# Kernel optimization log

Hardware: AMD Instinct MI355X
Metric: run time of the kernel (lower is better)

## Reference

```python
import jax, jax.numpy as jnp
import numpy as np

B, S, E, H = 2, 2048, 4096, 32
D = E // H  # head_dim = 128
MAX_SEQ = 2048


def precompute_freqs(dim, end, theta=10000.0):
    # Faithful to the torch source, including its operator precedence:
    # freqs = 1.0 / (theta ** arange(0, dim, 2)[:dim//2].float() / dim)
    # i.e. 1.0 / ((theta ** exps) / dim); overflows to inf in fp32 -> freq 0.
    exps = jnp.arange(0, dim, 2, dtype=jnp.float32)[: dim // 2]
    freqs = 1.0 / (jnp.power(jnp.float32(theta), exps) / jnp.float32(dim))
    t = jnp.arange(end, dtype=jnp.float32)
    f = jnp.outer(t, freqs)  # [end, dim//2]
    return jnp.cos(f), jnp.sin(f)


def apply_rope(x, cos, sin, pos):
    # x: [B,H,S,D]; cos/sin: [max_seq, dim//2]; pos: [B,S]
    c = cos[pos][:, None]  # [B,1,S,f]
    s = sin[pos][:, None]
    xr = x.reshape(*x.shape[:-1], -1, 2)  # [B,H,S,D/2,2]
    x1, x2 = xr[..., 0], xr[..., 1]
    if x1.shape[-1] > c.shape[-1]:
        rep = x1.shape[-1] // c.shape[-1]  # repeat_interleave factor
        c = jnp.repeat(c, rep, axis=-1)
        s = jnp.repeat(s, rep, axis=-1)
    out = jnp.stack([x1 * c - x2 * s, x1 * s + x2 * c], axis=-1)
    return out.reshape(x.shape)


def setup_inputs() -> dict:
    key = jax.random.key(0)
    kx, kq, kk, kv, ko = jax.random.split(key, 5)
    x = jax.random.normal(kx, (B, S, E), jnp.float32)
    scale = 0.02
    Wq = jax.random.normal(kq, (E, E), jnp.float32) * scale
    Wk = jax.random.normal(kk, (E, E), jnp.float32) * scale
    Wv = jax.random.normal(kv, (E, E), jnp.float32) * scale
    Wo = jax.random.normal(ko, (E, E), jnp.float32) * scale
    z = jnp.zeros((E,), jnp.float32)
    return {"x": x, "Wq": Wq, "bq": z, "Wk": Wk, "bk": z, "Wv": Wv, "bv": z, "Wo": Wo, "bo": z}


def reference(x, Wq, bq, Wk, bk, Wv, bv, Wo, bo):
    cos, sin = precompute_freqs(H, MAX_SEQ)  # note: dim = n_heads, as in source
    pos = jnp.broadcast_to(jnp.arange(S)[None, :], (B, S))  # no offset, S <= max
    # QKV projections (torch Linear: x @ W.T + b)
    q = (x @ Wq.T + bq).reshape(B, S, H, D).transpose(0, 2, 1, 3)  # [B,H,S,D]
    k = (x @ Wk.T + bk).reshape(B, S, H, D).transpose(0, 2, 1, 3)
    v = (x @ Wv.T + bv).reshape(B, S, H, D).transpose(0, 2, 1, 3)
    q = apply_rope(q, cos, sin, pos)
    k = apply_rope(k, cos, sin, pos)
    # SDPA with mask=None (non-causal, full attention)
    scores = jnp.einsum("bhqd,bhkd->bhqk", q, k) / np.float32(np.sqrt(D))
    att = jax.nn.softmax(scores, axis=-1)
    out = jnp.einsum("bhqk,bhkd->bhqd", att, v)
    out = out.transpose(0, 2, 1, 3).reshape(B, S, E)
    return out @ Wo.T + bo
```

## Files before the change

kernel.cpp:

```cpp
#include <hip/hip_runtime.h>
#include <math.h>

typedef _Float16 half8 __attribute__((ext_vector_type(8)));
typedef _Float16 half4 __attribute__((ext_vector_type(4)));
typedef __fp16 fp16x2 __attribute__((ext_vector_type(2)));
typedef float f32x4 __attribute__((ext_vector_type(4)));
typedef unsigned uint4v __attribute__((ext_vector_type(4)));

struct FreqT { float f[16]; };

__device__ __forceinline__ f32x4 mfma16(half8 a, half8 b, f32x4 c) {
  return __builtin_amdgcn_mfma_f32_16x16x32_f16(a, b, c, 0, 0, 0);
}

__device__ __forceinline__ void gload_lds16(const void* g, void* l) {
  __builtin_amdgcn_global_load_lds(
      (const __attribute__((address_space(1))) void*)g,
      (__attribute__((address_space(3))) void*)l, 16, 0, 0);
}

__device__ __forceinline__ unsigned pk_f16(float p0, float p1) {
  fp16x2 h = __builtin_amdgcn_cvt_pkrtz(p0, p1);
  return __builtin_bit_cast(unsigned, h);
}

#define S_BARRIER() __builtin_amdgcn_s_barrier()
#define WAIT_LGKM0() asm volatile("s_waitcnt lgkmcnt(0)" ::: "memory")
#define WAIT_VM8() asm volatile("s_waitcnt vmcnt(8)" ::: "memory")
#define WAIT_VM4() asm volatile("s_waitcnt vmcnt(4)" ::: "memory")
#define WAIT_VM0() asm volatile("s_waitcnt vmcnt(0)" ::: "memory")

__global__ __launch_bounds__(256)
void cast_f32_f16(const float* __restrict__ in, _Float16* __restrict__ out, long n8) {
  long i = (long)blockIdx.x * blockDim.x + threadIdx.x;
  if (i >= n8) return;
  float4 a = ((const float4*)in)[2 * i];
  float4 b = ((const float4*)in)[2 * i + 1];
  half8 v;
  v[0] = (_Float16)a.x; v[1] = (_Float16)a.y; v[2] = (_Float16)a.z; v[3] = (_Float16)a.w;
  v[4] = (_Float16)b.x; v[5] = (_Float16)b.y; v[6] = (_Float16)b.z; v[7] = (_Float16)b.w;
  ((half8*)out)[i] = v;
}

#define GBM 256
#define GBN 256
#define GBK 64

template <typename OutT>
__global__ __launch_bounds__(512, 2)
void gemm256(const _Float16* __restrict__ A, const _Float16* __restrict__ W,
             const float* __restrict__ bias, OutT* __restrict__ C,
             int M, int N, int K) {
  __shared__ __align__(16) _Float16 lds[4][GBM * GBK];

  int nwg = gridDim.x;
  int bid = blockIdx.x;
  int cpx = nwg >> 3;
  int swz = (bid & 7) * cpx + (bid >> 3);
  int ntn = N / GBN;
  int m0 = (swz / ntn) * GBM, n0 = (swz % ntn) * GBN;

  int tid = threadIdx.x, lane = tid & 63, w = tid >> 6;
  int wm = w >> 2, wn = w & 3;
  int g = lane >> 4, lc = lane & 15;

  int r8 = w * 8 + (lane >> 3);
  int cs = (((lane & 7) ^ (lane >> 3)) << 3);
  const _Float16* gA = A + (size_t)(m0 + r8) * K + cs;
  const _Float16* gB = W + (size_t)(n0 + r8) * K + cs;

#define STAGE(bi, k0) do {                                            \
    _Float16* la_ = &lds[(bi) * 2][0] + w * 512;                      \
    _Float16* lb_ = &lds[(bi) * 2 + 1][0] + w * 512;                  \
    _Pragma("unroll")                                                 \
    for (int i_ = 0; i_ < 4; ++i_) {                                  \
      gload_lds16(gA + (size_t)(i_ * 64) * K + (k0), la_ + i_ * 4096);\
      gload_lds16(gB + (size_t)(i_ * 64) * K + (k0), lb_ + i_ * 4096);\
    } } while (0)

  int aOff[8], bOff[4];
#pragma unroll
  for (int mf = 0; mf < 8; ++mf) aOff[mf] = (wm * 128 + mf * 16 + lc) * 64;
#pragma unroll
  for (int nf = 0; nf < 4; ++nf) bOff[nf] = (wn * 64 + nf * 16 + lc) * 64;
  int co0 = (((0 * 4 + g) ^ (lc & 7)) << 3);
  int co1 = (((1 * 4 + g) ^ (lc & 7)) << 3);

  half8 a0[8], a1[8], b0[4], b1[4];
  f32x4 acc[8][4] = {};

#define LOAD_SET0(bi) do {                                            \
    const _Float16* lA_ = &lds[(bi) * 2][0];                          \
    const _Float16* lB_ = &lds[(bi) * 2 + 1][0];                      \
    _Pragma("unroll")                                                 \
    for (int mf = 0; mf < 4; ++mf) {                                  \
      a0[mf * 2 + 0] = *(const half8*)&lA_[aOff[mf] + co0];           \
      a0[mf * 2 + 1] = *(const half8*)&lA_[aOff[mf] + co1];           \
    }                                                                 \
    _Pragma("unroll")                                                 \
    for (int nf = 0; nf < 2; ++nf) {                                  \
      b0[nf * 2 + 0] = *(const half8*)&lB_[bOff[nf] + co0];           \
      b0[nf * 2 + 1] = *(const half8*)&lB_[bOff[nf] + co1];           \
    } } while (0)

#define LOAD_SET1(bi) do {                                            \
    const _Float16* lA_ = &lds[(bi) * 2][0];                          \
    const _Float16* lB_ = &lds[(bi) * 2 + 1][0];                      \
    _Pragma("unroll")                                                 \
    for (int mf = 0; mf < 4; ++mf) {                                  \
      a1[mf * 2 + 0] = *(const half8*)&lA_[aOff[mf + 4] + co0];       \
      a1[mf * 2 + 1] = *(const half8*)&lA_[aOff[mf + 4] + co1];       \
    }                                                                 \
    _Pragma("unroll")                                                 \
    for (int nf = 0; nf < 2; ++nf) {                                  \
      b1[nf * 2 + 0] = *(const half8*)&lB_[bOff[nf + 2] + co0];       \
      b1[nf * 2 + 1] = *(const half8*)&lB_[bOff[nf + 2] + co1];       \
    } } while (0)

#define MFMA_Q(mq, nq, ar, br) do {                                   \
    __builtin_amdgcn_s_setprio(1);                                    \
    _Pragma("unroll")                                                 \
    for (int mf = 0; mf < 4; ++mf)                                    \
      _Pragma("unroll")                                               \
      for (int nf = 0; nf < 2; ++nf)                                  \
        _Pragma("unroll")                                             \
        for (int kk = 0; kk < 2; ++kk)                                \
          acc[(mq) * 4 + mf][(nq) * 2 + nf] =                         \
              mfma16(ar[mf * 2 + kk], br[nf * 2 + kk],                \
                     acc[(mq) * 4 + mf][(nq) * 2 + nf]);              \
    __builtin_amdgcn_s_setprio(0); } while (0)

  const int NT = K >> 6;

  STAGE(0, 0);
  STAGE(1, GBK);
  WAIT_VM8();
  S_BARRIER();
  LOAD_SET0(0);

  for (int t = 0; t < NT - 2; ++t) {
    int cur = t & 1;
    LOAD_SET1(cur);
    MFMA_Q(0, 0, a0, b0);
    MFMA_Q(0, 1, a0, b1);
    WAIT_LGKM0();
    S_BARRIER();
    STAGE(cur, (t + 2) << 6);
    MFMA_Q(1, 1, a1, b1);
    MFMA_Q(1, 0, a1, b0);
    WAIT_VM8();
    S_BARRIER();
    LOAD_SET0(cur ^ 1);
  }
  {
    int cur = (NT - 2) & 1;
    LOAD_SET1(cur);
    MFMA_Q(0, 0, a0, b0);
    MFMA_Q(0, 1, a0, b1);
    MFMA_Q(1, 1, a1, b1);
    MFMA_Q(1, 0, a1, b0);
    WAIT_VM0();
    S_BARRIER();
    LOAD_SET0(cur ^ 1);
  }
  {
    LOAD_SET1((NT - 1) & 1);
    MFMA_Q(0, 0, a0, b0);
    MFMA_Q(0, 1, a0, b1);
    MFMA_Q(1, 1, a1, b1);
    MFMA_Q(1, 0, a1, b0);
  }

  int crow = m0 + wm * 128 + g * 4;
  int ccol = n0 + wn * 64 + lc;
#pragma unroll
  for (int nf = 0; nf < 4; ++nf) {
    float bv = bias[ccol + nf * 16];
#pragma unroll
    for (int mf = 0; mf < 8; ++mf)
#pragma unroll
      for (int j = 0; j < 4; ++j)
        C[(size_t)(crow + mf * 16 + j) * N + ccol + nf * 16] =
            (OutT)(acc[mf][nf][j] + bv);
  }
#undef STAGE
#undef LOAD_SET0
#undef LOAD_SET1
#undef MFMA_Q
}

__global__ __launch_bounds__(256)
void rope_kernel(_Float16* __restrict__ x, FreqT ft, int Sn, int E, long n8) {
  long i = (long)blockIdx.x * blockDim.x + threadIdx.x;
  if (i >= n8) return;
  int epr = E / 8;
  int e8 = (int)(i % epr);
  int s = (int)((i / epr) % Sn);
  int fj = e8 & 15;
  float fr = ft.f[fj];
  float ang = (float)s * fr;
  float sv, cv;
  sincosf(ang, &sv, &cv);
  half8 v = ((const half8*)x)[i];
  half8 o;
#pragma unroll
  for (int p = 0; p < 4; ++p) {
    float x1 = (float)v[2 * p], x2 = (float)v[2 * p + 1];
    o[2 * p] = (_Float16)(x1 * cv - x2 * sv);
    o[2 * p + 1] = (_Float16)(x1 * sv + x2 * cv);
  }
  ((half8*)x)[i] = o;
}

__global__ __launch_bounds__(256)
void transpose_v(const _Float16* __restrict__ v, _Float16* __restrict__ vt,
                 int Hn, int Sn) {
  const int D = 128;
  const int E = Hn * D;
  __shared__ _Float16 t[64][130];
  int spb = Sn / 64;
  int bid = blockIdx.x;
  int s0 = (bid % spb) * 64;
  int bh = bid / spb;
  int b = bh / Hn, h = bh % Hn;
  int tid = threadIdx.x;
  int r = tid >> 2, dc = (tid & 3) * 32;
  const _Float16* src = v + (size_t)(b * Sn + s0 + r) * E + h * D + dc;
#pragma unroll
  for (int i = 0; i < 4; ++i) {
    half8 x = *(const half8*)(src + i * 8);
#pragma unroll
    for (int k = 0; k < 4; ++k) {
      _Float16 a0 = x[2 * k], a1 = x[2 * k + 1];
      t[r][dc + i * 8 + 2 * k] = a0;
      t[r][dc + i * 8 + 2 * k + 1] = a1;
    }
  }
  __syncthreads();
  int d = tid >> 1, sh = (tid & 1) * 32;
  half8 ov[4];
#pragma unroll
  for (int c = 0; c < 4; ++c)
#pragma unroll
    for (int j = 0; j < 8; ++j)
      ov[c][j] = t[sh + c * 8 + j][d];
  _Float16* dst = vt + ((size_t)bh * D + d) * Sn + s0 + sh;
#pragma unroll
  for (int c = 0; c < 4; ++c)
    *(half8*)(dst + c * 8) = ov[c];
}

#define QB 128
#define KB 64

__global__ __launch_bounds__(256, 2)
void flash_attn(const _Float16* __restrict__ qg, const _Float16* __restrict__ kg,
                const _Float16* __restrict__ vt, _Float16* __restrict__ og,
                int Bn, int Hn, int Sn) {
  const int D = 128;
  const int E = Hn * D;

  __shared__ _Float16 Ksh[2][KB * 128];
  __shared__ _Float16 Vsh[D * KB];
  __shared__ float sm[4][32];

  int qtiles = Sn / QB;
  int bid = blockIdx.x;
  int bh = bid / qtiles, qt = bid % qtiles;
  int b = bh / Hn, h = bh % Hn;

  int tid = threadIdx.x, lane = tid & 63, w = tid >> 6;
  int g = lane >> 4, lc = lane & 15;
  int lc7 = lc & 7;

  const size_t headoff = ((size_t)b * Sn) * E + (size_t)h * D;
  const _Float16* qp = qg + headoff;
  const _Float16* kp = kg + headoff;
  const _Float16* vtp = vt + (size_t)(b * Hn + h) * D * Sn;

  int q0 = qt * QB + w * 32;
  half8 aq[2][4];
#pragma unroll
  for (int mf = 0; mf < 2; ++mf)
#pragma unroll
    for (int kf = 0; kf < 4; ++kf)
      aq[mf][kf] = *(const half8*)(qp + (size_t)(q0 + mf * 16 + lc) * E + kf * 32 + g * 8);

  float mrun[2] = {-1e30f, -1e30f}, lpart[2] = {0.f, 0.f};
  f32x4 o[2][8] = {};

  const float scale = 0.08838834764831845f;

  int krow = 4 * w + (lane >> 4);
  int kcol = ((lane & 15) ^ (krow & 7)) * 8;
  const _Float16* gK = kp + (size_t)krow * E + kcol;
  int vrow = w * 32 + (lane >> 3);
  int vcol = ((lane & 7) ^ (vrow & 7)) * 8;
  const _Float16* gV = vtp + (size_t)vrow * Sn + vcol;

  float* smw = sm[w];

  const int NT = Sn / KB;

  {
    _Float16* lK = Ksh[0] + w * 512;
#pragma unroll
    for (int i = 0; i < 4; ++i)
      gload_lds16(gK + (size_t)(16 * i) * E, lK + i * 2048);
  }
  WAIT_VM0();
  S_BARRIER();

  for (int t = 0; t < NT; ++t) {
    int c = t & 1;
    {
      _Float16* lV = Vsh + w * 2048;
#pragma unroll
      for (int p = 0; p < 4; ++p)
        gload_lds16(gV + (size_t)(p * 8) * Sn + t * KB, lV + p * 512);
    }
    if (t + 1 < NT) {
      _Float16* lK = Ksh[c ^ 1] + w * 512;
#pragma unroll
      for (int i = 0; i < 4; ++i)
        gload_lds16(gK + (size_t)((t + 1) * KB + 16 * i) * E, lK + i * 2048);
    }

    f32x4 st[2][4] = {};
    {
      const _Float16* Kc = Ksh[c];
      __builtin_amdgcn_s_setprio(1);
#pragma unroll
      for (int kf = 0; kf < 4; ++kf) {
        half8 bk[4];
#pragma unroll
        for (int nf = 0; nf < 4; ++nf)
          bk[nf] = *(const half8*)&Kc[(nf * 16 + lc) * 128 + (((kf * 4 + g) ^ lc7) << 3)];
#pragma unroll
        for (int nf = 0; nf < 4; ++nf)
#pragma unroll
          for (int mf = 0; mf < 2; ++mf)
            st[mf][nf] = mfma16(bk[nf], aq[mf][kf], st[mf][nf]);
      }
      __builtin_amdgcn_s_setprio(0);
    }

    bool resc[2];
#pragma unroll
    for (int mf = 0; mf < 2; ++mf) {
      f32x4 m4 = st[mf][0];
#pragma unroll
      for (int nf = 1; nf < 4; ++nf)
#pragma unroll
        for (int j = 0; j < 4; ++j) m4[j] = fmaxf(m4[j], st[mf][nf][j]);
      float mx = fmaxf(fmaxf(m4[0], m4[1]), fmaxf(m4[2], m4[3]));
      mx = fmaxf(mx, __shfl_xor(mx, 16));
      mx = fmaxf(mx, __shfl_xor(mx, 32));
      mx *= scale;
      resc[mf] = __any(mx > mrun[mf] + 8.f);
      if (resc[mf]) {
        float mnew = fmaxf(mrun[mf], mx);
        float r = __expf(mrun[mf] - mnew);
        mrun[mf] = mnew;
        lpart[mf] *= r;
        if (g == 0) smw[mf * 16 + lc] = r;
      }
    }
#pragma unroll
    for (int mf = 0; mf < 2; ++mf)
      if (resc[mf]) {
        f32x4 rv = *(const f32x4*)&smw[mf * 16 + g * 4];
#pragma unroll
        for (int df = 0; df < 8; ++df)
#pragma unroll
          for (int j = 0; j < 4; ++j) o[mf][df][j] *= rv[j];
      }

    half8 pa00, pa01, pa10, pa11;
#define PACK_P(MF, PA0, PA1) do {                                          \
      float e0, e1;                                                        \
      e0 = __expf(st[MF][0][0] * scale - mrun[MF]);                        \
      e1 = __expf(st[MF][0][1] * scale - mrun[MF]);                        \
      lpart[MF] += e0 + e1; unsigned k00 = pk_f16(e0, e1);                 \
      e0 = __expf(st[MF][0][2] * scale - mrun[MF]);                        \
      e1 = __expf(st[MF][0][3] * scale - mrun[MF]);                        \
      lpart[MF] += e0 + e1; unsigned k01 = pk_f16(e0, e1);                 \
      e0 = __expf(st[MF][1][0] * scale - mrun[MF]);                        \
      e1 = __expf(st[MF][1][1] * scale - mrun[MF]);                        \
      lpart[MF] += e0 + e1; unsigned k10 = pk_f16(e0, e1);                 \
      e0 = __expf(st[MF][1][2] * scale - mrun[MF]);                        \
      e1 = __expf(st[MF][1][3] * scale - mrun[MF]);                        \
      lpart[MF] += e0 + e1; unsigned k11 = pk_f16(e0, e1);                 \
      e0 = __expf(st[MF][2][0] * scale - mrun[MF]);                        \
      e1 = __expf(st[MF][2][1] * scale - mrun[MF]);                        \
      lpart[MF] += e0 + e1; unsigned k20 = pk_f16(e0, e1);                 \
      e0 = __expf(st[MF][2][2] * scale - mrun[MF]);                        \
      e1 = __expf(st[MF][2][3] * scale - mrun[MF]);                        \
      lpart[MF] += e0 + e1; unsigned k21 = pk_f16(e0, e1);                 \
      e0 = __expf(st[MF][3][0] * scale - mrun[MF]);                        \
      e1 = __expf(st[MF][3][1] * scale - mrun[MF]);                        \
      lpart[MF] += e0 + e1; unsigned k30 = pk_f16(e0, e1);                 \
      e0 = __expf(st[MF][3][2] * scale - mrun[MF]);                        \
      e1 = __expf(st[MF][3][3] * scale - mrun[MF]);                        \
      lpart[MF] += e0 + e1; unsigned k31 = pk_f16(e0, e1);                 \
      asm("v_permlane32_swap_b32 %0, %1" : "+v"(k00), "+v"(k10));          \
      asm("v_permlane16_swap_b32 %0, %1" : "+v"(k00), "+v"(k10));          \
      asm("v_permlane32_swap_b32 %0, %1" : "+v"(k01), "+v"(k11));          \
      asm("v_permlane16_swap_b32 %0, %1" : "+v"(k01), "+v"(k11));          \
      asm("v_permlane32_swap_b32 %0, %1" : "+v"(k20), "+v"(k30));          \
      asm("v_permlane16_swap_b32 %0, %1" : "+v"(k20), "+v"(k30));          \
      asm("v_permlane32_swap_b32 %0, %1" : "+v"(k21), "+v"(k31));          \
      asm("v_permlane16_swap_b32 %0, %1" : "+v"(k21), "+v"(k31));          \
      uint4v p0v, p1v;                                                     \
      p0v[0] = k00; p0v[1] = k01; p0v[2] = k10; p0v[3] = k11;              \
      p1v[0] = k20; p1v[1] = k21; p1v[2] = k30; p1v[3] = k31;              \
      PA0 = __builtin_bit_cast(half8, p0v);                                \
      PA1 = __builtin_bit_cast(half8, p1v);                                \
    } while (0)
    PACK_P(0, pa00, pa01);
    PACK_P(1, pa10, pa11);
#undef PACK_P

    if (t + 1 < NT) { WAIT_VM4(); } else { WAIT_VM0(); }
    S_BARRIER();

    __builtin_amdgcn_s_setprio(1);
    {
      int csw0 = (g ^ lc7) << 3;
      int csw1 = ((4 + g) ^ lc7) << 3;
#pragma unroll
      for (int df = 0; df < 8; ++df) {
        half8 bv0 = *(const half8*)&Vsh[(df * 16 + lc) * 64 + csw0];
        o[0][df] = mfma16(pa00, bv0, o[0][df]);
        o[1][df] = mfma16(pa10, bv0, o[1][df]);
      }
#pragma unroll
      for (int df = 0; df < 8; ++df) {
        half8 bv1 = *(const half8*)&Vsh[(df * 16 + lc) * 64 + csw1];
        o[0][df] = mfma16(pa01, bv1, o[0][df]);
        o[1][df] = mfma16(pa11, bv1, o[1][df]);
      }
    }
    __builtin_amdgcn_s_setprio(0);

    if (t + 1 < NT) {
      WAIT_VM0();
      S_BARRIER();
    }
  }

#pragma unroll
  for (int mf = 0; mf < 2; ++mf) {
    float l = lpart[mf];
    l += __shfl_xor(l, 16);
    l += __shfl_xor(l, 32);
    if (g == 0) smw[mf * 16 + lc] = 1.0f / l;
  }
  _Float16* op = og + headoff;
#pragma unroll
  for (int mf = 0; mf < 2; ++mf) {
    f32x4 li = *(const f32x4*)&smw[mf * 16 + g * 4];
#pragma unroll
    for (int j = 0; j < 4; ++j) {
      int row = q0 + mf * 16 + g * 4 + j;
#pragma unroll
      for (int df = 0; df < 8; ++df)
        op[(size_t)row * E + df * 16 + lc] = (_Float16)(o[mf][df][j] * li[j]);
    }
  }
}

extern "C" void kernel_launch(void* const* d_in, const int* in_sizes, int n_in,
                              void* d_out, int out_size, void* d_ws, size_t ws_size,
                              hipStream_t stream) {
  const float* x  = (const float*)d_in[0];
  const float* Wq = (const float*)d_in[1];
  const float* bq = (const float*)d_in[2];
  const float* Wk = (const float*)d_in[3];
  const float* bk = (const float*)d_in[4];
  const float* Wv = (const float*)d_in[5];
  const float* bv = (const float*)d_in[6];
  const float* Wo = (const float*)d_in[7];
  const float* bo = (const float*)d_in[8];

  const int E = in_sizes[2];
  const int M = in_sizes[0] / E;
  const int S = 2048;
  const int Bb = M / S;
  const int H = 32;

  _Float16* xh = (_Float16*)d_ws;
  _Float16* wh = xh + (size_t)M * E;
  _Float16* qh = wh + (size_t)E * E;
  _Float16* kh = qh + (size_t)M * E;
  _Float16* vh = kh + (size_t)M * E;
  _Float16* oh = xh;
  _Float16* vtb = wh;

  FreqT ft;
  for (int j = 0; j < 16; ++j) {
    float pf = (float)pow(10000.0, (double)(2 * j));
    ft.f[j] = 1.0f / (pf / 32.0f);
  }

  long nx8 = (long)M * E / 8;
  long nw8 = (long)E * E / 8;
  dim3 blk(256);
  int cb_x = (int)((nx8 + 255) / 256);
  int cb_w = (int)((nw8 + 255) / 256);
  int gemm_grid = (M / GBM) * (E / GBN);

  cast_f32_f16<<<cb_x, blk, 0, stream>>>(x, xh, nx8);

  cast_f32_f16<<<cb_w, blk, 0, stream>>>(Wq, wh, nw8);
  gemm256<_Float16><<<gemm_grid, 512, 0, stream>>>(xh, wh, bq, qh, M, E, E);
  cast_f32_f16<<<cb_w, blk, 0, stream>>>(Wk, wh, nw8);
  gemm256<_Float16><<<gemm_grid, 512, 0, stream>>>(xh, wh, bk, kh, M, E, E);
  cast_f32_f16<<<cb_w, blk, 0, stream>>>(Wv, wh, nw8);
  gemm256<_Float16><<<gemm_grid, 512, 0, stream>>>(xh, wh, bv, vh, M, E, E);

  rope_kernel<<<cb_x, blk, 0, stream>>>(qh, ft, S, E, nx8);
  rope_kernel<<<cb_x, blk, 0, stream>>>(kh, ft, S, E, nx8);

  transpose_v<<<Bb * H * (S / 64), blk, 0, stream>>>(vh, vtb, H, S);

  flash_attn<<<Bb * H * (S / QB), blk, 0, stream>>>(qh, kh, vtb, oh, Bb, H, S);

  cast_f32_f16<<<cb_w, blk, 0, stream>>>(Wo, wh, nw8);
  gemm256<float><<<gemm_grid, 512, 0, stream>>>(oh, wh, bo, (float*)d_out, M, E, E);
}
```

Baseline: 773.1 us.

## Double-buffer V, prefetch K two tiles ahead, swizzle blocks across XCDs

Gives the flash-attention kernel a double-buffered V tile in LDS and issues K loads two tiles ahead. The tail barrier of each iteration goes away, so global-to-LDS copies overlap both the QK^T and PV MFMA phases instead of blocking between iterations. It also remaps block IDs so that consecutive blocks on the same XCD share a head, which is meant to improve L2 reuse of K/V. The cost is more LDS per block, which could limit occupancy, and a more delicate wait-count and barrier protocol.

```diff
diff --git a/kernel.cpp b/kernel.cpp
--- a/kernel.cpp
+++ b/kernel.cpp
@@ -261,12 +261,14 @@
   const int E = Hn * D;
 
   __shared__ _Float16 Ksh[2][KB * 128];
-  __shared__ _Float16 Vsh[D * KB];
+  __shared__ _Float16 Vsh[2][D * KB];
   __shared__ float sm[4][32];
 
   int qtiles = Sn / QB;
+  int nwg = gridDim.x;
   int bid = blockIdx.x;
-  int bh = bid / qtiles, qt = bid % qtiles;
+  int swzb = (bid & 7) * (nwg >> 3) + (bid >> 3);
+  int bh = swzb / qtiles, qt = swzb % qtiles;
   int b = bh / Hn, h = bh % Hn;
 
   int tid = threadIdx.x, lane = tid & 63, w = tid >> 6;
@@ -302,29 +304,27 @@
 
   const int NT = Sn / KB;
 
-  {
-    _Float16* lK = Ksh[0] + w * 512;
-#pragma unroll
-    for (int i = 0; i < 4; ++i)
-      gload_lds16(gK + (size_t)(16 * i) * E, lK + i * 2048);
-  }
-  WAIT_VM0();
+#define STAGE_K(buf, kt) do {                                          \
+    _Float16* lK_ = Ksh[buf] + w * 512;                                \
+    _Pragma("unroll")                                                  \
+    for (int i_ = 0; i_ < 4; ++i_)                                     \
+      gload_lds16(gK + (size_t)((kt) * KB + 16 * i_) * E, lK_ + i_ * 2048); \
+  } while (0)
+#define STAGE_V(buf, kt) do {                                          \
+    _Float16* lV_ = Vsh[buf] + w * 2048;                               \
+    _Pragma("unroll")                                                  \
+    for (int p_ = 0; p_ < 4; ++p_)                                     \
+      gload_lds16(gV + (size_t)(p_ * 8) * Sn + (kt) * KB, lV_ + p_ * 512); \
+  } while (0)
+
+  STAGE_K(0, 0);
+  STAGE_K(1, 1);
+  STAGE_V(0, 0);
+  WAIT_VM8();
   S_BARRIER();
 
   for (int t = 0; t < NT; ++t) {
     int c = t & 1;
-    {
-      _Float16* lV = Vsh + w * 2048;
-#pragma unroll
-      for (int p = 0; p < 4; ++p)
-        gload_lds16(gV + (size_t)(p * 8) * Sn + t * KB, lV + p * 512);
-    }
-    if (t + 1 < NT) {
-      _Float16* lK = Ksh[c ^ 1] + w * 512;
-#pragma unroll
-      for (int i = 0; i < 4; ++i)
-        gload_lds16(gK + (size_t)((t + 1) * KB + 16 * i) * E, lK + i * 2048);
-    }
 
     f32x4 st[2][4] = {};
     {
@@ -344,6 +344,11 @@
       }
       __builtin_amdgcn_s_setprio(0);
     }
+    WAIT_LGKM0();
+    S_BARRIER();
+
+    if (t + 1 < NT) STAGE_V(c ^ 1, t + 1);
+    if (t + 2 < NT) STAGE_K(c, t + 2);
 
     bool resc[2];
 #pragma unroll
@@ -421,33 +426,33 @@
     PACK_P(1, pa10, pa11);
 #undef PACK_P
 
-    if (t + 1 < NT) { WAIT_VM4(); } else { WAIT_VM0(); }
+    if (t + 2 < NT) { WAIT_VM8(); }
+    else if (t + 1 < NT) { WAIT_VM4(); }
+    else { WAIT_VM0(); }
     S_BARRIER();
 
     __builtin_amdgcn_s_setprio(1);
     {
+      const _Float16* Vc = Vsh[c];
       int csw0 = (g ^ lc7) << 3;
       int csw1 = ((4 + g) ^ lc7) << 3;
 #pragma unroll
       for (int df = 0; df < 8; ++df) {
-        half8 bv0 = *(const half8*)&Vsh[(df * 16 + lc) * 64 + csw0];
+        half8 bv0 = *(const half8*)&Vc[(df * 16 + lc) * 64 + csw0];
         o[0][df] = mfma16(pa00, bv0, o[0][df]);
         o[1][df] = mfma16(pa10, bv0, o[1][df]);
       }
 #pragma unroll
       for (int df = 0; df < 8; ++df) {
-        half8 bv1 = *(const half8*)&Vsh[(df * 16 + lc) * 64 + csw1];
+        half8 bv1 = *(const half8*)&Vc[(df * 16 + lc) * 64 + csw1];
         o[0][df] = mfma16(pa01, bv1, o[0][df]);
         o[1][df] = mfma16(pa11, bv1, o[1][df]);
       }
     }
     __builtin_amdgcn_s_setprio(0);
-
-    if (t + 1 < NT) {
-      WAIT_VM0();
-      S_BARRIER();
-    }
-  }
+  }
+#undef STAGE_K
+#undef STAGE_V
 
 #pragma unroll
   for (int mf = 0; mf < 2; ++mf) {
```

Measured after the change: 763.7 us. About the same (-1.2%).
